# Performance work log

Measured on AMD Instinct MI355X. Metric: run time of the kernel, lower is better.

## Reference

```python
import math
import jax, jax.numpy as jnp
import numpy as np

D_MODEL = 1024
N_HEADS = 16
HEAD_DIM = 64          # block_size
NUM_RULES = 64
RANK = 8               # proj_rank = round(sqrt(head_dim)); also router_rank
SHARED_RANK = 32       # round(sqrt(d_model))
NUM_BLOCKS = 16        # min(in,out)//block_size = 1024//64; total_block_dim == d_model
B, S = 4, 1024
ROPE_BASE = 10000.0


def setup_inputs() -> dict:
    key = jax.random.key(0)
    ks = iter(jax.random.split(key, 32))
    def nrm(shape, s=0.02):
        return jax.random.normal(next(ks), shape, dtype=jnp.float32) * s
    inp = {
        "x": jax.random.normal(next(ks), (B, S, D_MODEL), dtype=jnp.float32),
        "target_rule_ids": jax.random.randint(next(ks), (B, S), 0, NUM_RULES),
    }
    for p in ("q", "k", "v", "o"):
        inp[p + "_si"] = nrm((D_MODEL, SHARED_RANK))
        inp[p + "_so"] = nrm((SHARED_RANK, D_MODEL))
        inp[p + "_ri"] = nrm((NUM_RULES, HEAD_DIM, RANK))
        inp[p + "_ro"] = nrm((NUM_RULES, RANK, HEAD_DIM))
        inp[p + "_lg"] = nrm((NUM_RULES, NUM_BLOCKS), 1.0 / math.sqrt(NUM_BLOCKS))
    inp["router_q"] = nrm((NUM_RULES, RANK))
    inp["router_k"] = nrm((NUM_RULES, RANK))
    return inp


def _rule_proj(x, rules, si, so, ri, ro, lg):
    """RuleAwareProjection.forward_rules_batched, de-permuted.

    The torch code argsorts tokens by rule, zero-pads per-rule buckets, runs
    bmm per rule and scatters back; mathematically that equals a per-token
    gather of the rule's low-rank adapter, which is what we compute here.
    x: [N, D_MODEL], rules: [N] int.
    """
    base = (x @ si) @ so                                  # shared low-rank path
    xb = x.reshape(-1, NUM_BLOCKS, HEAD_DIM)              # [N, nb, bs]
    h = jnp.einsum('nbs,nsr->nbr', xb, ri[rules])         # [N, nb, rank]
    a = jnp.einsum('nbr,nrt->nbt', h, ro[rules])          # [N, nb, bs]
    # temperature = 1/sqrt(num_blocks) => logits / temperature = logits*sqrt(nb)
    sel = jax.nn.softmax(lg[rules] * math.sqrt(NUM_BLOCKS), axis=-1)
    return base + (a * sel[:, :, None]).reshape(-1, D_MODEL)


def _rope(q, k):
    # q, k: [B, H, S, D]; interleaved-pair rotation, start_pos = 0.
    S_, D = q.shape[2], q.shape[3]
    pos = jnp.arange(S_, dtype=jnp.float32)[:, None]
    div = jnp.exp(jnp.arange(0, D, 2, dtype=jnp.float32) * (-math.log(ROPE_BASE) / D))
    f = pos * div                                         # [S, D/2]
    sin, cos = jnp.sin(f), jnp.cos(f)
    def rot(t):
        t1, t2 = t[..., 0::2], t[..., 1::2]
        return jnp.stack([t1 * cos - t2 * sin, t2 * cos + t1 * sin], axis=-1).reshape(t.shape)
    return rot(q), rot(k)


def reference(x, target_rule_ids,
              q_si, q_so, q_ri, q_ro, q_lg,
              k_si, k_so, k_ri, k_ro, k_lg,
              v_si, v_so, v_ri, v_ro, v_lg,
              o_si, o_so, o_ri, o_ro, o_lg,
              router_q, router_k):
    B_, S_, C = x.shape
    flat_x = x.reshape(-1, C)
    rules = target_rule_ids.reshape(-1)

    q = _rule_proj(flat_x, rules, q_si, q_so, q_ri, q_ro, q_lg)
    k = _rule_proj(flat_x, rules, k_si, k_so, k_ri, k_ro, k_lg)
    v = _rule_proj(flat_x, rules, v_si, v_so, v_ri, v_ro, v_lg)
    q = q.reshape(B_, S_, N_HEADS, HEAD_DIM).transpose(0, 2, 1, 3)
    k = k.reshape(B_, S_, N_HEADS, HEAD_DIM).transpose(0, 2, 1, 3)
    v = v.reshape(B_, S_, N_HEADS, HEAD_DIM).transpose(0, 2, 1, 3)
    q, k = _rope(q, k)

    # rule-routing sparse mask: cosine affinity between token rule embeddings
    rq = router_q[target_rule_ids]                        # [B, S, rank]
    rk = router_k[target_rule_ids]
    rqn = rq / jnp.maximum(jnp.linalg.norm(rq, axis=-1, keepdims=True), 1e-12)
    rkn = rk / jnp.maximum(jnp.linalg.norm(rk, axis=-1, keepdims=True), 1e-12)
    tau = 1.0 / math.log(max(math.e, RANK))
    aff = jnp.einsum('bqr,bkr->bqk', rqn, rkn) / tau       # [B, S, S]
    causal = jnp.tril(jnp.ones((S_, S_), dtype=bool))
    masked = jnp.where(causal[None], aff, -jnp.inf)
    top_k = max(2, int(math.sqrt(S_)))
    if S_ > top_k:
        thr = jax.lax.top_k(masked, top_k)[0][..., -1:]
        rule_mask = (masked >= thr) & causal[None]
    else:
        rule_mask = jnp.broadcast_to(causal[None], masked.shape)

    scores = jnp.einsum('bhqd,bhkd->bhqk', q, k) / math.sqrt(HEAD_DIM)
    scores = jnp.where(rule_mask[:, None], scores, -jnp.inf)
    attn = jax.nn.softmax(scores, axis=-1)
    out = jnp.einsum('bhqk,bhkd->bhqd', attn, v)
    out = out.transpose(0, 2, 1, 3).reshape(-1, C)
    out = _rule_proj(out, rules, o_si, o_so, o_ri, o_ro, o_lg)
    return out.reshape(B_, S_, C)
```

## Files before the change

### kernel.cpp

```cpp
#include <hip/hip_runtime.h>
#include <hip/hip_bf16.h>

#define D_MODEL 1024
#define N_HEADS 16
#define HEAD_DIM 64
#define NUM_RULES 64
#define RANK 8
#define SHARED_RANK 32
#define NUM_BLOCKS_ 16
#define BB 4
#define SS 1024
#define NTOK (BB*SS)
#define NGRP (NTOK/8)
#define NGRP4 (NTOK/4)

typedef __attribute__((ext_vector_type(8))) short bf16x8;
typedef __attribute__((ext_vector_type(4))) float f32x4;

__device__ __forceinline__ float bf2f(unsigned short u) {
  unsigned int i = ((unsigned int)u) << 16;
  float f;
  __builtin_memcpy(&f, &i, 4);
  return f;
}
__device__ __forceinline__ unsigned short f2bf(float f) {
  __hip_bfloat16 h = __float2bfloat16(f);
  unsigned short u;
  __builtin_memcpy(&u, &h, 2);
  return u;
}
__device__ __forceinline__ float u2f(unsigned int i) {
  float f;
  __builtin_memcpy(&f, &i, 4);
  return f;
}
template<bool BF>
__device__ __forceinline__ float ldw(const void* p, size_t i) {
  if (BF) return bf2f(((const unsigned short*)p)[i]);
  else    return ((const float*)p)[i];
}

__device__ __forceinline__ void gload16(const void* g, void* l) {
  __builtin_amdgcn_global_load_lds(
      (const __attribute__((address_space(1))) unsigned int*)g,
      (__attribute__((address_space(3))) unsigned int*)l, 16, 0, 0);
}

__global__ void detect_kernel(const unsigned short* __restrict__ x, int* __restrict__ flag) {
  const int lane = threadIdx.x;
  int good = 0;
  for (int i = 0; i < 4; i++) {
    unsigned short u = x[lane*4 + i];
    int e = (u >> 7) & 0xFF;
    good += (e == 0 || (e >= 100 && e <= 145)) ? 1 : 0;
  }
  for (int off = 32; off; off >>= 1) good += __shfl_xor(good, off);
  if (lane == 0) flag[0] = (good >= 224) ? 1 : 0;
}

template<bool BF>
__device__ __forceinline__ void precompute_body(
    const void* rq, const void* rk,
    const void* qlg, const void* klg, const void* vlg, const void* olg,
    float* __restrict__ M, float* __restrict__ sel)
{
  __shared__ float rqn[64][8], rkn[64][8];
  const int tid = threadIdx.x;
  if (tid < 64) {
    float v[8]; float s = 0.f;
    for (int i = 0; i < 8; i++) { v[i] = ldw<BF>(rq, tid*8+i); s += v[i]*v[i]; }
    float inv = 1.0f / fmaxf(sqrtf(s), 1e-12f);
    for (int i = 0; i < 8; i++) rqn[tid][i] = v[i]*inv;
  } else if (tid < 128) {
    int r = tid - 64;
    float v[8]; float s = 0.f;
    for (int i = 0; i < 8; i++) { v[i] = ldw<BF>(rk, r*8+i); s += v[i]*v[i]; }
    float inv = 1.0f / fmaxf(sqrtf(s), 1e-12f);
    for (int i = 0; i < 8; i++) rkn[r][i] = v[i]*inv;
  }
  __syncthreads();
  const float LN8 = 2.0794415416798357f;
  for (int idx = tid; idx < 64*64; idx += 256) {
    int i = idx >> 6, j = idx & 63;
    float d = 0.f;
    for (int t = 0; t < 8; t++) d += rqn[i][t]*rkn[j][t];
    M[idx] = d * LN8;
  }
  const void* lgs[4] = {qlg, klg, vlg, olg};
  {
    int r = tid & 63;
    const void* lg = lgs[tid >> 6];
    float e[NUM_BLOCKS_]; float mx = -1e30f;
    for (int b = 0; b < NUM_BLOCKS_; b++) {
      e[b] = ldw<BF>(lg, r*NUM_BLOCKS_ + b) * 4.0f;
      mx = fmaxf(mx, e[b]);
    }
    float s = 0.f;
    for (int b = 0; b < NUM_BLOCKS_; b++) { e[b] = expf(e[b]-mx); s += e[b]; }
    float inv = 1.0f/s;
    for (int b = 0; b < NUM_BLOCKS_; b++) sel[tid*NUM_BLOCKS_+b] = e[b]*inv;
  }
}

__global__ void precompute_kernel(
    const void* rq, const void* rk,
    const void* qlg, const void* klg, const void* vlg, const void* olg,
    float* M, float* sel, const int* __restrict__ flag)
{
  if (*flag) precompute_body<true >(rq, rk, qlg, klg, vlg, olg, M, sel);
  else       precompute_body<false>(rq, rk, qlg, klg, vlg, olg, M, sel);
}

template<bool IN_BF, bool W_BF>
__device__ __forceinline__ void stageA_body(
    const void* __restrict__ xin, const int* __restrict__ rules,
    const void* __restrict__ si, const void* __restrict__ ri,
    float* __restrict__ ttg, float* __restrict__ hhg, int yslot)
{
  const int g = blockIdx.x, n0 = g*8, tid = threadIdx.x;
  __shared__ float xs[8][D_MODEL];
  __shared__ float tpart[8][32][9];
  __shared__ int rl[8];

  #pragma unroll
  for (int t = 0; t < 8; t++) {
    float4 f;
    if (IN_BF) {
      ushort4 u = ((const ushort4*)((const unsigned short*)xin + (size_t)(n0+t)*D_MODEL))[tid];
      f.x = bf2f(u.x); f.y = bf2f(u.y); f.z = bf2f(u.z); f.w = bf2f(u.w);
    } else {
      f = ((const float4*)xin)[(size_t)(n0+t)*(D_MODEL/4) + tid];
    }
    *(float4*)&xs[t][tid*4] = f;
  }
  if (tid < 8) rl[tid] = rules[n0 + tid];
  __syncthreads();

  {
    const int c = tid >> 5, j = tid & 31;
    float p[8];
    #pragma unroll
    for (int t = 0; t < 8; t++) p[t] = 0.f;
    #pragma unroll 4
    for (int d4 = 0; d4 < 32; d4++) {
      const int d = c*128 + d4*4;
      float w0 = ldw<W_BF>(si, (size_t)(d+0)*SHARED_RANK + j);
      float w1 = ldw<W_BF>(si, (size_t)(d+1)*SHARED_RANK + j);
      float w2 = ldw<W_BF>(si, (size_t)(d+2)*SHARED_RANK + j);
      float w3 = ldw<W_BF>(si, (size_t)(d+3)*SHARED_RANK + j);
      #pragma unroll
      for (int t = 0; t < 8; t++) {
        float4 xv = *(const float4*)&xs[t][d];
        p[t] += xv.x*w0 + xv.y*w1 + xv.z*w2 + xv.w*w3;
      }
    }
    #pragma unroll
    for (int t = 0; t < 8; t++) tpart[c][j][t] = p[t];
  }
  __syncthreads();

  {
    const int t = tid >> 5, j = tid & 31;
    float s = 0.f;
    #pragma unroll
    for (int c = 0; c < 8; c++) s += tpart[c][j][t];
    ttg[(size_t)(yslot*NGRP + g)*256 + j*8 + t] = s;
  }
  {
    const int t = tid >> 5, blk = (tid >> 1) & 15, r0 = (tid & 1)*4;
    const int rule = rl[t];
    float a0=0.f, a1=0.f, a2=0.f, a3=0.f;
    #pragma unroll 4
    for (int k4 = 0; k4 < 16; k4++) {
      const int kk = ((k4 + blk) & 15) * 4;
      float4 xv = *(const float4*)&xs[t][blk*64 + kk];
      #pragma unroll
      for (int q = 0; q < 4; q++) {
        const int k = kk + q;
        float w0,w1,w2,w3;
        if (W_BF) {
          ushort4 u = *(const ushort4*)((const unsigned short*)ri + (size_t)rule*512 + (size_t)k*8 + r0);
          w0=bf2f(u.x); w1=bf2f(u.y); w2=bf2f(u.z); w3=bf2f(u.w);
        } else {
          float4 u = *(const float4*)((const float*)ri + (size_t)rule*512 + (size_t)k*8 + r0);
          w0=u.x; w1=u.y; w2=u.z; w3=u.w;
        }
        float xq = (q==0)?xv.x:((q==1)?xv.y:((q==2)?xv.z:xv.w));
        a0 += xq*w0; a1 += xq*w1; a2 += xq*w2; a3 += xq*w3;
      }
    }
    float4 hv; hv.x=a0; hv.y=a1; hv.z=a2; hv.w=a3;
    *(float4*)&hhg[((size_t)yslot*NTOK + n0 + t)*128 + blk*8 + r0] = hv;
  }
}

__global__ __launch_bounds__(256) void A_qkv_bf16(
    const void* x, const int* rules,
    const void* qsi, const void* qri, const void* ksi, const void* kri,
    const void* vsi, const void* vri,
    float* ttg, float* hhg, const int* __restrict__ flag)
{
  if (!*flag) return;
  const int y = blockIdx.y;
  const void* si = (y==0)?qsi:((y==1)?ksi:vsi);
  const void* ri = (y==0)?qri:((y==1)?kri:vri);
  stageA_body<true,true>(x, rules, si, ri, ttg, hhg, y);
}

__global__ __launch_bounds__(256) void A_qkv_f32(
    const void* x, const int* rules,
    const void* qsi, const void* qri, const void* ksi, const void* kri,
    const void* vsi, const void* vri,
    float* ttg, float* hhg, const int* __restrict__ flag)
{
  if (*flag) return;
  const int y = blockIdx.y;
  const void* si = (y==0)?qsi:((y==1)?ksi:vsi);
  const void* ri = (y==0)?qri:((y==1)?kri:vri);
  stageA_body<false,false>(x, rules, si, ri, ttg, hhg, y);
}

__global__ __launch_bounds__(256) void A_o_bf16(
    const void* ain, const int* rules, const void* osi, const void* ori,
    float* ttg, float* hhg, const int* __restrict__ flag)
{
  if (!*flag) return;
  stageA_body<false,true>(ain, rules, osi, ori, ttg, hhg, 0);
}

template<bool W_BF>
__device__ __forceinline__ void stageB_body(
    const float* __restrict__ ttg, const float* __restrict__ hhg,
    const int* __restrict__ rules,
    const void* __restrict__ so, const void* __restrict__ ro,
    const float* __restrict__ sel, void* __restrict__ out,
    int yslot, int do_rope, int out_bf)
{
  const int blk4 = blockIdx.x;
  const int g8 = blk4 >> 1, half = blk4 & 1;
  const int n0 = blk4*4, tid = threadIdx.x;
  __shared__ float tt_lds[32][5];
  __shared__ float hh_lds[4][132];
  __shared__ int rl[4];

  if (tid < 128) {
    const int j = tid >> 2, t4 = tid & 3;
    tt_lds[j][t4] = ttg[(size_t)(yslot*NGRP + g8)*256 + j*8 + half*4 + t4];
  } else if (tid < 256 && (tid - 128) < 128) {
    const int i = tid - 128;
    const int t4 = i >> 5, c = (i*4) & 127;
    float4 hv = *(const float4*)&hhg[((size_t)yslot*NTOK + n0 + t4)*128 + c];
    *(float4*)&hh_lds[t4][c] = hv;
  }
  if (tid < 4) rl[tid] = rules[n0 + tid];
  __syncthreads();

  const int ch0 = tid*4;
  float a0[4], a1[4], a2[4], a3[4];
  #pragma unroll
  for (int t = 0; t < 4; t++) { a0[t]=0.f; a1[t]=0.f; a2[t]=0.f; a3[t]=0.f; }

  #pragma unroll 4
  for (int j = 0; j < 32; j++) {
    float w0, w1, w2, w3;
    if (W_BF) {
      ushort4 u = *(const ushort4*)((const unsigned short*)so + (size_t)j*D_MODEL + ch0);
      w0=bf2f(u.x); w1=bf2f(u.y); w2=bf2f(u.z); w3=bf2f(u.w);
    } else {
      float4 u = *(const float4*)((const float*)so + (size_t)j*D_MODEL + ch0);
      w0=u.x; w1=u.y; w2=u.z; w3=u.w;
    }
    #pragma unroll
    for (int t = 0; t < 4; t++) {
      float tv = tt_lds[j][t];
      a0[t] += tv*w0; a1[t] += tv*w1; a2[t] += tv*w2; a3[t] += tv*w3;
    }
  }

  const int blk = ch0 >> 6, tc = ch0 & 63;
  float inv0 = 0.f, inv1 = 0.f;
  if (do_rope) {
    inv0 = expf(-(float)tc     * (9.210340371976184f/64.0f));
    inv1 = expf(-(float)(tc+2) * (9.210340371976184f/64.0f));
  }
  #pragma unroll 2
  for (int t = 0; t < 4; t++) {
    const int rule = rl[t];
    float b0=0.f, b1=0.f, b2=0.f, b3=0.f;
    #pragma unroll
    for (int r = 0; r < 8; r++) {
      float w0,w1,w2,w3;
      if (W_BF) {
        ushort4 u = *(const ushort4*)((const unsigned short*)ro + (size_t)rule*512 + r*64 + tc);
        w0=bf2f(u.x); w1=bf2f(u.y); w2=bf2f(u.z); w3=bf2f(u.w);
      } else {
        float4 u = *(const float4*)((const float*)ro + (size_t)rule*512 + r*64 + tc);
        w0=u.x; w1=u.y; w2=u.z; w3=u.w;
      }
      float hv = hh_lds[t][blk*8 + r];
      b0 += hv*w0; b1 += hv*w1; b2 += hv*w2; b3 += hv*w3;
    }
    float sb = sel[rule*NUM_BLOCKS_ + blk];
    float e0 = a0[t] + b0*sb, o0 = a1[t] + b1*sb;
    float e1 = a2[t] + b2*sb, o1 = a3[t] + b3*sb;
    const int n = n0 + t;
    if (do_rope) {
      float spos = (float)(n & (SS-1));
      float sn0, cs0, sn1, cs1;
      sincosf(spos*inv0, &sn0, &cs0);
      sincosf(spos*inv1, &sn1, &cs1);
      float u0 = e0*cs0 - o0*sn0; o0 = o0*cs0 + e0*sn0; e0 = u0;
      float u1 = e1*cs1 - o1*sn1; o1 = o1*cs1 + e1*sn1; e1 = u1;
    }
    if (out_bf) {
      ushort4 uv; uv.x=f2bf(e0); uv.y=f2bf(o0); uv.z=f2bf(e1); uv.w=f2bf(o1);
      *(ushort4*)((unsigned short*)out + (size_t)n*D_MODEL + ch0) = uv;
    } else {
      float4 fv; fv.x=e0; fv.y=o0; fv.z=e1; fv.w=o1;
      *(float4*)((float*)out + (size_t)n*D_MODEL + ch0) = fv;
    }
  }
}

__global__ __launch_bounds__(256) void B_qkv_bf16(
    const float* ttg, const float* hhg, const int* rules,
    const void* qso, const void* qro, const void* kso, const void* kro,
    const void* vso, const void* vro,
    const float* sel, float* qb, unsigned short* kb, unsigned short* vb,
    const int* __restrict__ flag)
{
  if (!*flag) return;
  const int y = blockIdx.y;
  const void* so = (y==0)?qso:((y==1)?kso:vso);
  const void* ro = (y==0)?qro:((y==1)?kro:vro);
  void* out = (y==0)?(void*)qb:((y==1)?(void*)kb:(void*)vb);
  stageB_body<true>(ttg, hhg, rules, so, ro, sel + y*1024, out, y, (y<2)?1:0, (y>=1)?1:0);
}

__global__ __launch_bounds__(256) void B_qkv_f32(
    const float* ttg, const float* hhg, const int* rules,
    const void* qso, const void* qro, const void* kso, const void* kro,
    const void* vso, const void* vro,
    const float* sel, float* qb, unsigned short* kb, unsigned short* vb,
    const int* __restrict__ flag)
{
  if (*flag) return;
  const int y = blockIdx.y;
  const void* so = (y==0)?qso:((y==1)?kso:vso);
  const void* ro = (y==0)?qro:((y==1)?kro:vro);
  void* out = (y==0)?(void*)qb:((y==1)?(void*)kb:(void*)vb);
  stageB_body<false>(ttg, hhg, rules, so, ro, sel + y*1024, out, y, (y<2)?1:0, (y>=1)?1:0);
}

__global__ __launch_bounds__(256) void B_o_bf16(
    const float* ttg, const float* hhg, const int* rules,
    const void* oso, const void* oro, const float* sel, void* out,
    const int* __restrict__ flag)
{
  if (!*flag) return;
  stageB_body<true>(ttg, hhg, rules, oso, oro, sel, out, 0, 0, 1);
}

__global__ __launch_bounds__(256) void B_o_f32(
    const float* ttg, const float* hhg, const int* rules,
    const void* oso, const void* oro, const float* sel, void* out,
    const int* __restrict__ flag)
{
  if (*flag) return;
  stageB_body<false>(ttg, hhg, rules, oso, oro, sel, out, 0, 0, 0);
}

__global__ __launch_bounds__(64) void mask_kernel(
    const int* __restrict__ rules, const float* __restrict__ M,
    unsigned long long* __restrict__ am)
{
  const int bid = blockIdx.x;
  const int b = bid >> 10, qi = bid & 1023;
  const int lane = threadIdx.x;
  __shared__ int rrow[SS];
  __shared__ float val[64];
  __shared__ int cnth[64];
  for (int i = lane; i < SS/4; i += 64)
    ((int4*)rrow)[i] = ((const int4*)(rules + b*SS))[i];
  cnth[lane] = 0;
  __syncthreads();
  for (int k = lane; k <= qi; k += 64) atomicAdd(&cnth[rrow[k]], 1);
  const int qrule = rrow[qi];
  const float myv = M[qrule*64 + lane];
  val[lane] = myv;
  __syncthreads();
  const int c = cnth[lane];
  int A = 0;
  for (int r = 0; r < 64; r++) {
    int cr = __shfl(c, r);
    A += (val[r] > myv) ? cr : 0;
  }
  unsigned long long allowed = __ballot(A < 32);
  if (lane == 0) am[bid] = allowed;
}

__global__ __launch_bounds__(256) void vtrans_kernel(
    const unsigned short* __restrict__ vb, unsigned short* __restrict__ vt)
{
  const int st = blockIdx.x, h = blockIdx.y, b = blockIdx.z;
  __shared__ unsigned short t[64][72];
  const int tid = threadIdx.x;
  #pragma unroll
  for (int it = 0; it < 2; it++) {
    int i = tid + it*256;
    int r = i >> 3, c8 = (i & 7)*8;
    uint4 v = *(const uint4*)(vb + ((size_t)(b*SS + st*64 + r)*D_MODEL + h*HEAD_DIM + c8));
    t[c8+0][r] = (unsigned short)(v.x & 0xffffu);
    t[c8+1][r] = (unsigned short)(v.x >> 16);
    t[c8+2][r] = (unsigned short)(v.y & 0xffffu);
    t[c8+3][r] = (unsigned short)(v.y >> 16);
    t[c8+4][r] = (unsigned short)(v.z & 0xffffu);
    t[c8+5][r] = (unsigned short)(v.z >> 16);
    t[c8+6][r] = (unsigned short)(v.w & 0xffffu);
    t[c8+7][r] = (unsigned short)(v.w >> 16);
  }
  __syncthreads();
  #pragma unroll
  for (int it = 0; it < 2; it++) {
    int i = tid + it*256;
    int d = i >> 3, c8 = i & 7;
    uint4 o = *(const uint4*)&t[d][c8*8];
    *(uint4*)(vt + ((size_t)(b*N_HEADS + h)*HEAD_DIM + d)*SS + st*64 + c8*8) = o;
  }
}

__global__ __launch_bounds__(256) void attn_mfma_kernel(
    const float* __restrict__ qb,
    const unsigned short* __restrict__ kb,
    const unsigned short* __restrict__ vtb,
    const int* __restrict__ rules,
    const unsigned long long* __restrict__ am,
    float* outb)
{
  const int qx = blockIdx.x, b = blockIdx.y, h = blockIdx.z;
  const int tid = threadIdx.x, lane = tid & 63, w = tid >> 6;
  __shared__ unsigned short Ks[2][64*64];
  __shared__ unsigned short Vs[2][64*64];
  __shared__ unsigned short Pl[4][16*64];
  __shared__ int rl[SS];

  ((int4*)rl)[tid] = ((const int4*)(rules + b*SS))[tid];

  const unsigned short* kbase = kb + (size_t)b*SS*D_MODEL + h*HEAD_DIM;
  const unsigned short* vbase = vtb + (size_t)(b*N_HEADS + h)*HEAD_DIM*SS;

  const int srow0 = tid >> 3;
  const int spos  = tid & 7;
  unsigned short* pw = &Pl[w][0];

  for (int halfq = 0; halfq < 2; halfq++) {
    const int qt = halfq ? (15 - qx) : qx;

    const int qa = qt*64 + w*16 + (lane & 15);
    bf16x8 qfrag[2];
    {
      const float* qrow = qb + (size_t)(b*SS + qa)*D_MODEL + h*HEAD_DIM + (lane>>4)*8;
      #pragma unroll
      for (int kc = 0; kc < 2; kc++) {
        float4 f0 = *(const float4*)(qrow + kc*32);
        float4 f1 = *(const float4*)(qrow + kc*32 + 4);
        bf16x8 qv;
        qv[0] = (short)f2bf(f0.x*0.125f); qv[1] = (short)f2bf(f0.y*0.125f);
        qv[2] = (short)f2bf(f0.z*0.125f); qv[3] = (short)f2bf(f0.w*0.125f);
        qv[4] = (short)f2bf(f1.x*0.125f); qv[5] = (short)f2bf(f1.y*0.125f);
        qv[6] = (short)f2bf(f1.z*0.125f); qv[7] = (short)f2bf(f1.w*0.125f);
        qfrag[kc] = qv;
      }
    }
    int qg[4]; unsigned aqlo[4], aqhi[4];
    #pragma unroll
    for (int r = 0; r < 4; r++) {
      qg[r] = qt*64 + w*16 + (lane>>4)*4 + r;
      uint2 mm = *(const uint2*)(am + (size_t)b*SS + qg[r]);
      aqlo[r] = mm.x; aqhi[r] = mm.y;
    }
    f32x4 Oacc[4];
    #pragma unroll
    for (int nt = 0; nt < 4; nt++) Oacc[nt] = (f32x4){0.f,0.f,0.f,0.f};
    float mrun[4], lrun[4];
    #pragma unroll
    for (int r = 0; r < 4; r++) { mrun[r] = -1e30f; lrun[r] = 0.f; }

    #pragma unroll
    for (int it = 0; it < 2; it++) {
      int row = srow0 + it*32;
      int sc = spos ^ (row & 7);
      gload16(kbase + (size_t)row*D_MODEL + sc*8, &Ks[0][(row*8 + spos)*8]);
      gload16(vbase + (size_t)row*SS + sc*8,      &Vs[0][(row*8 + spos)*8]);
    }
    __syncthreads();

    int cur = 0;
    for (int kt = 0; kt <= qt; kt++) {
      if (kt < qt) {
        const size_t koff = (size_t)(kt + 1)*64;
        #pragma unroll
        for (int it = 0; it < 2; it++) {
          int row = srow0 + it*32;
          int sc = spos ^ (row & 7);
          gload16(kbase + (koff + row)*D_MODEL + sc*8, &Ks[cur^1][(row*8 + spos)*8]);
          gload16(vbase + (size_t)row*SS + koff + sc*8, &Vs[cur^1][(row*8 + spos)*8]);
        }
      }
      const unsigned short* kt_lds = Ks[cur];
      const unsigned short* vt_lds = Vs[cur];

      f32x4 Sacc[4];
      #pragma unroll
      for (int nt = 0; nt < 4; nt++) {
        const int key = nt*16 + (lane & 15);
        f32x4 c = (f32x4){0.f,0.f,0.f,0.f};
        #pragma unroll
        for (int kc = 0; kc < 2; kc++) {
          int off = (key*128 + kc*64 + (lane>>4)*16) ^ ((key & 7) << 4);
          bf16x8 kf = *(const bf16x8*)((const char*)kt_lds + off);
          c = __builtin_amdgcn_mfma_f32_16x16x32_bf16(qfrag[kc], kf, c, 0, 0, 0);
        }
        Sacc[nt] = c;
      }

      float sv[4][4];
      #pragma unroll
      for (int nt = 0; nt < 4; nt++) {
        const int k = kt*64 + nt*16 + (lane & 15);
        const int rr = rl[k];
        const unsigned sh = (unsigned)rr & 31u;
        const bool hi = rr >= 32;
        #pragma unroll
        for (int r = 0; r < 4; r++) {
          unsigned bits = hi ? aqhi[r] : aqlo[r];
          bool ok = (((bits >> sh) & 1u) != 0u) && (k <= qg[r]);
          sv[nt][r] = ok ? Sacc[nt][r] : -3e38f;
        }
      }

      float tm[4];
      #pragma unroll
      for (int r = 0; r < 4; r++)
        tm[r] = fmaxf(fmaxf(sv[0][r], sv[1][r]), fmaxf(sv[2][r], sv[3][r]));
      #pragma unroll
      for (int off = 1; off < 16; off <<= 1) {
        #pragma unroll
        for (int r = 0; r < 4; r++) tm[r] = fmaxf(tm[r], __shfl_xor(tm[r], off));
      }
      float alpha[4];
      #pragma unroll
      for (int r = 0; r < 4; r++) {
        float nm = fmaxf(mrun[r], tm[r]);
        alpha[r] = __expf(mrun[r] - nm);
        mrun[r] = nm;
      }
      float ps[4] = {0.f, 0.f, 0.f, 0.f};
      #pragma unroll
      for (int nt = 0; nt < 4; nt++) {
        #pragma unroll
        for (int r = 0; r < 4; r++) {
          float p = __expf(sv[nt][r] - mrun[r]);
          ps[r] += p;
          const int q = (lane>>4)*4 + r;
          int off = (q*128 + (nt*16 + (lane & 15))*2) ^ ((q & 7) << 4);
          *(unsigned short*)((char*)pw + off) = f2bf(p);
        }
      }
      #pragma unroll
      for (int off = 1; off < 16; off <<= 1) {
        #pragma unroll
        for (int r = 0; r < 4; r++) ps[r] += __shfl_xor(ps[r], off);
      }
      #pragma unroll
      for (int r = 0; r < 4; r++) lrun[r] = lrun[r]*alpha[r] + ps[r];
      #pragma unroll
      for (int nt = 0; nt < 4; nt++) {
        Oacc[nt][0] *= alpha[0]; Oacc[nt][1] *= alpha[1];
        Oacc[nt][2] *= alpha[2]; Oacc[nt][3] *= alpha[3];
      }

      #pragma unroll
      for (int kc = 0; kc < 2; kc++) {
        const int qrow = lane & 15;
        int aoff = (qrow*128 + kc*64 + (lane>>4)*16) ^ ((qrow & 7) << 4);
        bf16x8 pa = *(const bf16x8*)((const char*)pw + aoff);
        #pragma unroll
        for (int nt = 0; nt < 4; nt++) {
          const int d = nt*16 + (lane & 15);
          int boff = (d*128 + kc*64 + (lane>>4)*16) ^ ((d & 7) << 4);
          bf16x8 vf = *(const bf16x8*)((const char*)vt_lds + boff);
          Oacc[nt] = __builtin_amdgcn_mfma_f32_16x16x32_bf16(pa, vf, Oacc[nt], 0, 0, 0);
        }
      }
      __syncthreads();
      cur ^= 1;
    }

    float invl[4];
    #pragma unroll
    for (int r = 0; r < 4; r++) invl[r] = 1.0f / lrun[r];
    #pragma unroll
    for (int nt = 0; nt < 4; nt++) {
      #pragma unroll
      for (int r = 0; r < 4; r++) {
        outb[(size_t)(b*SS + qg[r])*D_MODEL + h*HEAD_DIM + nt*16 + (lane & 15)]
            = Oacc[nt][r]*invl[r];
      }
    }
  }
}

extern "C" void kernel_launch(void* const* d_in, const int* in_sizes, int n_in,
                              void* d_out, int out_size, void* d_ws, size_t ws_size,
                              hipStream_t stream) {
  (void)in_sizes; (void)n_in; (void)out_size; (void)ws_size;
  const void* x    = d_in[0];
  const int* rules = (const int*)d_in[1];
  const void* q_si = d_in[2];  const void* q_so = d_in[3];
  const void* q_ri = d_in[4];  const void* q_ro = d_in[5];  const void* q_lg = d_in[6];
  const void* k_si = d_in[7];  const void* k_so = d_in[8];
  const void* k_ri = d_in[9];  const void* k_ro = d_in[10]; const void* k_lg = d_in[11];
  const void* v_si = d_in[12]; const void* v_so = d_in[13];
  const void* v_ri = d_in[14]; const void* v_ro = d_in[15]; const void* v_lg = d_in[16];
  const void* o_si = d_in[17]; const void* o_so = d_in[18];
  const void* o_ri = d_in[19]; const void* o_ro = d_in[20]; const void* o_lg = d_in[21];
  const void* rq   = d_in[22]; const void* rk   = d_in[23];

  char* ws = (char*)d_ws;
  const size_t MB = 1024*1024;
  float*          qb    = (float*)(ws);
  unsigned short* kb    = (unsigned short*)(ws + 16*MB);
  unsigned short* vb    = (unsigned short*)(ws + 24*MB);
  unsigned short* vtb   = (unsigned short*)(ws + 32*MB);
  float*          ttg   = (float*)(ws + 40*MB);
  float*          hhg   = (float*)(ws + 42*MB);
  unsigned long long* amask = (unsigned long long*)(ws + 48*MB);
  float*          Mt    = (float*)(ws + 49*MB + 16*1024);
  float*          selt  = (float*)(ws + 49*MB + 32*1024);
  int*            flag  = (int*)  (ws + 49*MB + 48*1024);

  detect_kernel<<<1, 64, 0, stream>>>((const unsigned short*)x, flag);
  precompute_kernel<<<1, 256, 0, stream>>>(rq, rk, q_lg, k_lg, v_lg, o_lg, Mt, selt, flag);
  mask_kernel<<<NTOK, 64, 0, stream>>>(rules, Mt, amask);

  A_qkv_bf16<<<dim3(NGRP, 3), 256, 0, stream>>>(x, rules, q_si, q_ri, k_si, k_ri, v_si, v_ri, ttg, hhg, flag);
  A_qkv_f32 <<<dim3(NGRP, 3), 256, 0, stream>>>(x, rules, q_si, q_ri, k_si, k_ri, v_si, v_ri, ttg, hhg, flag);
  B_qkv_bf16<<<dim3(NGRP4, 3), 256, 0, stream>>>(ttg, hhg, rules, q_so, q_ro, k_so, k_ro, v_so, v_ro,
                                                 selt, qb, kb, vb, flag);
  B_qkv_f32 <<<dim3(NGRP4, 3), 256, 0, stream>>>(ttg, hhg, rules, q_so, q_ro, k_so, k_ro, v_so, v_ro,
                                                 selt, qb, kb, vb, flag);

  vtrans_kernel<<<dim3(16, 16, 4), 256, 0, stream>>>(vb, vtb);
  attn_mfma_kernel<<<dim3(8, BB, N_HEADS), 256, 0, stream>>>(qb, kb, vtb, rules, amask, qb);

  A_o_bf16<<<dim3(NGRP, 1), 256, 0, stream>>>(qb, rules, o_si, o_ri, ttg, hhg, flag);
  A_qkv_f32<<<dim3(NGRP, 1), 256, 0, stream>>>(qb, rules, o_si, o_ri, o_si, o_ri, o_si, o_ri, ttg, hhg, flag);
  B_o_bf16<<<NGRP4, 256, 0, stream>>>(ttg, hhg, rules, o_so, o_ro, selt + 3*1024, d_out, flag);
  B_o_f32 <<<NGRP4, 256, 0, stream>>>(ttg, hhg, rules, o_so, o_ro, selt + 3*1024, d_out, flag);
}
```

Measured before the change: 295.4 us.

## Split fp32 stage-A into split-bf16 MFMA shared projection and separate rule-adapter kernel

On the fp32 input path, the shared low-rank projection x@si now runs on MFMA using a three-term hi/lo bf16 split, which approximates fp32 accuracy. A prep kernel packs the si weights into MFMA-friendly hi/lo layouts, and the q/k/v variant processes all three projections in one pass over x. The per-rule adapter h computation moves to its own kernel that reads x straight from global memory and handles q, k and v together. The ttg layout changes to a token-major form, with the consumers updated to match. The trade is extra launches and weight prep for fewer scalar FMAs, with a small loss of precision from dropping the lo*lo term.

```diff
diff --git a/kernel.cpp b/kernel.cpp
--- a/kernel.cpp
+++ b/kernel.cpp
@@ -111,6 +111,175 @@
   else       precompute_body<false>(rq, rk, qlg, klg, vlg, olg, M, sel);
 }
 
+__global__ __launch_bounds__(128) void prep_wb_kernel(
+    const float* __restrict__ qsi, const float* __restrict__ ksi,
+    const float* __restrict__ vsi, const float* __restrict__ osi,
+    unsigned short* __restrict__ wh, unsigned short* __restrict__ wl,
+    const int* __restrict__ flag)
+{
+  if (*flag) return;
+  const int kt = blockIdx.x, p = blockIdx.y;
+  const int tid = threadIdx.x, nt = tid >> 6, lane = tid & 63;
+  const float* si = (p==0)?qsi:((p==1)?ksi:((p==2)?vsi:osi));
+  const int col = nt*16 + (lane & 15);
+  const int k0 = kt*32 + (lane >> 4)*8;
+  size_t base = ((((size_t)p*32 + kt)*2 + nt)*64 + lane)*8;
+  unsigned short h8[8], l8[8];
+  #pragma unroll
+  for (int j = 0; j < 8; j++) {
+    float f = si[(size_t)(k0 + j)*SHARED_RANK + col];
+    unsigned short hu = f2bf(f);
+    h8[j] = hu;
+    l8[j] = f2bf(f - bf2f(hu));
+  }
+  #pragma unroll
+  for (int j = 0; j < 8; j++) { wh[base + j] = h8[j]; wl[base + j] = l8[j]; }
+}
+
+template<int NPROJ>
+__device__ __forceinline__ void tt_mfma_body(
+    const float* __restrict__ xin,
+    const unsigned short* __restrict__ wh, const unsigned short* __restrict__ wl,
+    int p0, float* __restrict__ ttg)
+{
+  const int NT = NPROJ*2;
+  const int tile = blockIdx.x;
+  const int tid = threadIdx.x, lane = tid & 63, w = tid >> 6;
+  const int kq = lane >> 4;
+  __shared__ float red[4][64][25];
+
+  f32x4 acc[NT];
+  #pragma unroll
+  for (int i = 0; i < NT; i++) acc[i] = (f32x4){0.f,0.f,0.f,0.f};
+
+  const float* xrow = xin + (size_t)(tile*16 + (lane & 15))*D_MODEL + kq*8;
+  #pragma unroll 2
+  for (int s = 0; s < 8; s++) {
+    const int kt = w*8 + s;
+    float4 a0 = *(const float4*)(xrow + kt*32);
+    float4 a1 = *(const float4*)(xrow + kt*32 + 4);
+    float av[8] = {a0.x,a0.y,a0.z,a0.w,a1.x,a1.y,a1.z,a1.w};
+    bf16x8 ah, al;
+    #pragma unroll
+    for (int j = 0; j < 8; j++) {
+      unsigned short hu = f2bf(av[j]);
+      ah[j] = (short)hu;
+      al[j] = (short)f2bf(av[j] - bf2f(hu));
+    }
+    #pragma unroll
+    for (int p = 0; p < NPROJ; p++) {
+      #pragma unroll
+      for (int nt = 0; nt < 2; nt++) {
+        size_t bidx = ((((size_t)(p0+p)*32 + kt)*2 + nt)*64 + lane)*8;
+        bf16x8 bh = *(const bf16x8*)(wh + bidx);
+        bf16x8 bl = *(const bf16x8*)(wl + bidx);
+        f32x4 c = acc[p*2+nt];
+        c = __builtin_amdgcn_mfma_f32_16x16x32_bf16(ah, bh, c, 0, 0, 0);
+        c = __builtin_amdgcn_mfma_f32_16x16x32_bf16(al, bh, c, 0, 0, 0);
+        c = __builtin_amdgcn_mfma_f32_16x16x32_bf16(ah, bl, c, 0, 0, 0);
+        acc[p*2+nt] = c;
+      }
+    }
+  }
+  #pragma unroll
+  for (int i = 0; i < NT; i++) {
+    red[w][lane][i*4+0] = acc[i][0]; red[w][lane][i*4+1] = acc[i][1];
+    red[w][lane][i*4+2] = acc[i][2]; red[w][lane][i*4+3] = acc[i][3];
+  }
+  __syncthreads();
+  if (w == 0) {
+    const int tok0 = tile*16 + (lane >> 4)*4;
+    #pragma unroll
+    for (int i = 0; i < NT; i++) {
+      const int ys = i >> 1, jj = (i & 1)*16 + (lane & 15);
+      #pragma unroll
+      for (int r = 0; r < 4; r++) {
+        float sum = red[0][lane][i*4+r] + red[1][lane][i*4+r]
+                  + red[2][lane][i*4+r] + red[3][lane][i*4+r];
+        ttg[((size_t)ys*NTOK + tok0 + r)*32 + jj] = sum;
+      }
+    }
+  }
+}
+
+__global__ __launch_bounds__(256) void A_tt_mfma3(
+    const float* __restrict__ xin,
+    const unsigned short* __restrict__ wh, const unsigned short* __restrict__ wl,
+    float* __restrict__ ttg, const int* __restrict__ flag)
+{
+  if (*flag) return;
+  tt_mfma_body<3>(xin, wh, wl, 0, ttg);
+}
+
+__global__ __launch_bounds__(256) void A_tt_mfma1(
+    const float* __restrict__ xin,
+    const unsigned short* __restrict__ wh, const unsigned short* __restrict__ wl,
+    float* __restrict__ ttg, const int* __restrict__ flag)
+{
+  if (*flag) return;
+  tt_mfma_body<1>(xin, wh, wl, 3, ttg);
+}
+
+template<int NP>
+__device__ __forceinline__ void hh_body(
+    const float* __restrict__ xin, const int* __restrict__ rules,
+    const float* __restrict__ ri0, const float* __restrict__ ri1,
+    const float* __restrict__ ri2, float* __restrict__ hhg)
+{
+  const int g = blockIdx.x, n0 = g*8, tid = threadIdx.x;
+  const int t = tid >> 5, blk = (tid >> 1) & 15, r0 = (tid & 1)*4;
+  const int n = n0 + t;
+  const int rule = rules[n];
+  const float* xb = xin + (size_t)n*D_MODEL + blk*64;
+  const float* wb[3];
+  wb[0] = ri0 + (size_t)rule*512 + r0;
+  if (NP > 1) {
+    wb[1] = ri1 + (size_t)rule*512 + r0;
+    wb[2] = ri2 + (size_t)rule*512 + r0;
+  }
+  float a[NP][4];
+  #pragma unroll
+  for (int p = 0; p < NP; p++) { a[p][0]=0.f; a[p][1]=0.f; a[p][2]=0.f; a[p][3]=0.f; }
+  #pragma unroll 4
+  for (int k4 = 0; k4 < 16; k4++) {
+    float4 xv = *(const float4*)(xb + k4*4);
+    #pragma unroll
+    for (int q = 0; q < 4; q++) {
+      const int k = k4*4 + q;
+      float xq = (q==0)?xv.x:((q==1)?xv.y:((q==2)?xv.z:xv.w));
+      #pragma unroll
+      for (int p = 0; p < NP; p++) {
+        float4 wv = *(const float4*)(wb[p] + (size_t)k*8);
+        a[p][0] += xq*wv.x; a[p][1] += xq*wv.y; a[p][2] += xq*wv.z; a[p][3] += xq*wv.w;
+      }
+    }
+  }
+  #pragma unroll
+  for (int p = 0; p < NP; p++) {
+    float4 hv; hv.x=a[p][0]; hv.y=a[p][1]; hv.z=a[p][2]; hv.w=a[p][3];
+    *(float4*)&hhg[((size_t)p*NTOK + n)*128 + blk*8 + r0] = hv;
+  }
+}
+
+__global__ __launch_bounds__(256) void A_hh3_f32(
+    const float* __restrict__ xin, const int* __restrict__ rules,
+    const float* __restrict__ qri, const float* __restrict__ kri,
+    const float* __restrict__ vri, float* __restrict__ hhg,
+    const int* __restrict__ flag)
+{
+  if (*flag) return;
+  hh_body<3>(xin, rules, qri, kri, vri, hhg);
+}
+
+__global__ __launch_bounds__(256) void A_hh1_f32(
+    const float* __restrict__ xin, const int* __restrict__ rules,
+    const float* __restrict__ ori, float* __restrict__ hhg,
+    const int* __restrict__ flag)
+{
+  if (*flag) return;
+  hh_body<1>(xin, rules, ori, ori, ori, hhg);
+}
+
 template<bool IN_BF, bool W_BF>
 __device__ __forceinline__ void stageA_body(
     const void* __restrict__ xin, const int* __restrict__ rules,
@@ -164,7 +333,7 @@
     float s = 0.f;
     #pragma unroll
     for (int c = 0; c < 8; c++) s += tpart[c][j][t];
-    ttg[(size_t)(yslot*NGRP + g)*256 + j*8 + t] = s;
+    ttg[((size_t)yslot*NTOK + n0 + t)*32 + j] = s;
   }
   {
     const int t = tid >> 5, blk = (tid >> 1) & 15, r0 = (tid & 1)*4;
@@ -207,19 +376,6 @@
   stageA_body<true,true>(x, rules, si, ri, ttg, hhg, y);
 }
 
-__global__ __launch_bounds__(256) void A_qkv_f32(
-    const void* x, const int* rules,
-    const void* qsi, const void* qri, const void* ksi, const void* kri,
-    const void* vsi, const void* vri,
-    float* ttg, float* hhg, const int* __restrict__ flag)
-{
-  if (*flag) return;
-  const int y = blockIdx.y;
-  const void* si = (y==0)?qsi:((y==1)?ksi:vsi);
-  const void* ri = (y==0)?qri:((y==1)?kri:vri);
-  stageA_body<false,false>(x, rules, si, ri, ttg, hhg, y);
-}
-
 __global__ __launch_bounds__(256) void A_o_bf16(
     const void* ain, const int* rules, const void* osi, const void* ori,
     float* ttg, float* hhg, const int* __restrict__ flag)
@@ -237,7 +393,6 @@
     int yslot, int do_rope, int out_bf)
 {
   const int blk4 = blockIdx.x;
-  const int g8 = blk4 >> 1, half = blk4 & 1;
   const int n0 = blk4*4, tid = threadIdx.x;
   __shared__ float tt_lds[32][5];
   __shared__ float hh_lds[4][132];
@@ -245,7 +400,7 @@
 
   if (tid < 128) {
     const int j = tid >> 2, t4 = tid & 3;
-    tt_lds[j][t4] = ttg[(size_t)(yslot*NGRP + g8)*256 + j*8 + half*4 + t4];
+    tt_lds[j][t4] = ttg[((size_t)yslot*NTOK + n0 + t4)*32 + j];
   } else if (tid < 256 && (tid - 128) < 128) {
     const int i = tid - 128;
     const int t4 = i >> 5, c = (i*4) & 127;
@@ -639,13 +794,21 @@
   float*          Mt    = (float*)(ws + 49*MB + 16*1024);
   float*          selt  = (float*)(ws + 49*MB + 32*1024);
   int*            flag  = (int*)  (ws + 49*MB + 48*1024);
+  unsigned short* wpkh  = (unsigned short*)(ws + 49*MB + 64*1024);
+  unsigned short* wpkl  = (unsigned short*)(ws + 49*MB + 64*1024 + 256*1024);
 
   detect_kernel<<<1, 64, 0, stream>>>((const unsigned short*)x, flag);
   precompute_kernel<<<1, 256, 0, stream>>>(rq, rk, q_lg, k_lg, v_lg, o_lg, Mt, selt, flag);
   mask_kernel<<<NTOK, 64, 0, stream>>>(rules, Mt, amask);
+  prep_wb_kernel<<<dim3(32, 4), 128, 0, stream>>>(
+      (const float*)q_si, (const float*)k_si, (const float*)v_si, (const float*)o_si,
+      wpkh, wpkl, flag);
 
   A_qkv_bf16<<<dim3(NGRP, 3), 256, 0, stream>>>(x, rules, q_si, q_ri, k_si, k_ri, v_si, v_ri, ttg, hhg, flag);
-  A_qkv_f32 <<<dim3(NGRP, 3), 256, 0, stream>>>(x, rules, q_si, q_ri, k_si, k_ri, v_si, v_ri, ttg, hhg, flag);
+  A_tt_mfma3<<<256, 256, 0, stream>>>((const float*)x, wpkh, wpkl, ttg, flag);
+  A_hh3_f32<<<NGRP, 256, 0, stream>>>((const float*)x, rules,
+      (const float*)q_ri, (const float*)k_ri, (const float*)v_ri, hhg, flag);
+
   B_qkv_bf16<<<dim3(NGRP4, 3), 256, 0, stream>>>(ttg, hhg, rules, q_so, q_ro, k_so, k_ro, v_so, v_ro,
                                                  selt, qb, kb, vb, flag);
   B_qkv_f32 <<<dim3(NGRP4, 3), 256, 0, stream>>>(ttg, hhg, rules, q_so, q_ro, k_so, k_ro, v_so, v_ro,
@@ -655,7 +818,8 @@
   attn_mfma_kernel<<<dim3(8, BB, N_HEADS), 256, 0, stream>>>(qb, kb, vtb, rules, amask, qb);
 
   A_o_bf16<<<dim3(NGRP, 1), 256, 0, stream>>>(qb, rules, o_si, o_ri, ttg, hhg, flag);
-  A_qkv_f32<<<dim3(NGRP, 1), 256, 0, stream>>>(qb, rules, o_si, o_ri, o_si, o_ri, o_si, o_ri, ttg, hhg, flag);
+  A_tt_mfma1<<<256, 256, 0, stream>>>(qb, wpkh, wpkl, ttg, flag);
+  A_hh1_f32<<<NGRP, 256, 0, stream>>>(qb, rules, (const float*)o_ri, hhg, flag);
   B_o_bf16<<<NGRP4, 256, 0, stream>>>(ttg, hhg, rules, o_so, o_ro, selt + 3*1024, d_out, flag);
   B_o_f32 <<<NGRP4, 256, 0, stream>>>(ttg, hhg, rules, o_so, o_ro, selt + 3*1024, d_out, flag);
 }
```

After: 275.5 us. 1.07x faster.
